# Kernel tuning notes

Measured on AMD Instinct MI355X. Metric: run time of the kernel, lower is better.

## Reference

```python
import jax, jax.numpy as jnp
import numpy as np

B, C, V, L = 64, 32, 1024, 12
C_OUT = 64
ORDER = 2
C_CAT = (ORDER * 3 + 1) * C  # 224


def setup_inputs() -> dict:
    key = jax.random.key(0)
    ks = jax.random.split(key, 6)
    x = jax.random.normal(ks[0], (B, C, V, L), dtype=jnp.float32)
    # random non-negative adjacencies, row-normalized like diffusion supports
    def adj(k):
        a = jax.random.uniform(k, (V, V), dtype=jnp.float32)
        return a / jnp.sum(a, axis=1, keepdims=True)
    a0, a1, a2 = adj(ks[1]), adj(ks[2]), adj(ks[3])
    W = jax.random.normal(ks[4], (C_OUT, C_CAT), dtype=jnp.float32) * 0.05
    b = jax.random.normal(ks[5], (C_OUT,), dtype=jnp.float32) * 0.05
    return {"x": x, "a0": a0, "a1": a1, "a2": a2, "W": W, "b": b}


def reference(x, a0, a1, a2, W, b):
    # diffusion propagation: x[b,c,v,l] @ A[v,w] -> [b,c,w,l]
    def prop(z, A):
        return jnp.einsum('ncvl,vw->ncwl', z, A)

    out = [x]
    for A in (a0, a1, a2):
        x1 = prop(x, A)
        out.append(x1)
        x2 = prop(x1, A)  # order=2
        out.append(x2)
    h = jnp.concatenate(out, axis=1)  # [B, 7*C, V, L]
    # 1x1 conv == channel GEMM; dropout is identity at inference
    return jnp.einsum('ncvl,oc->novl', h, W) + b[None, :, None, None]
```

## Files before the change

### kernel.cpp

```cpp
#include <hip/hip_runtime.h>
#include <hip/hip_bf16.h>


typedef __attribute__((ext_vector_type(4))) float  f32x4;
typedef __attribute__((ext_vector_type(8))) short  s16x8;
typedef __attribute__((ext_vector_type(4))) short  s16x4;

__device__ inline short f2bf(float f) {
    unsigned u = __builtin_bit_cast(unsigned, f);
    unsigned r = (u + 0x7FFFu + ((u >> 16) & 1u)) >> 16;
    return (short)r;
}

__device__ inline f32x4 mfma16(s16x8 a, s16x8 b, f32x4 c) {
    return __builtin_amdgcn_mfma_f32_16x16x32_bf16(a, b, c, 0, 0, 0);
}

__device__ inline void gll16(const void* g, void* l) {
    __builtin_amdgcn_global_load_lds(
        (const __attribute__((address_space(1))) void*)g,
        (__attribute__((address_space(3))) void*)l, 16, 0, 0);
}

__global__ __launch_bounds__(256) void cast_x_v2(const float* __restrict__ x,
                                                 short* __restrict__ Xg) {
    __shared__ short Xl[12 * 1040];
    const int bc = blockIdx.x;
    const int t  = threadIdx.x;
    const float4* src = (const float4*)(x + (size_t)bc * 12288);
#pragma unroll
    for (int k = 0; k < 12; ++k) {
        int f4 = k * 256 + t;
        float4 v = src[f4];
        int f  = f4 * 4;
        int vi = f / 12;
        int li = f - vi * 12;
        float vals[4] = {v.x, v.y, v.z, v.w};
#pragma unroll
        for (int e = 0; e < 4; ++e) {
            Xl[li * 1040 + vi] = f2bf(vals[e]);
            if (++li == 12) { li = 0; ++vi; }
        }
    }
    __syncthreads();
#pragma unroll
    for (int k = 0; k < 6; ++k) {
        int ch = k * 256 + t;
        int l  = ch >> 7;
        int v8 = ch & 127;
        *(s16x8*)(Xg + ((size_t)bc * 12 + l) * 1024 + v8 * 8) =
            *(const s16x8*)&Xl[l * 1040 + v8 * 8];
    }
}

__global__ __launch_bounds__(256) void cast_a_v2(const float* __restrict__ a0,
                                                 const float* __restrict__ a1,
                                                 const float* __restrict__ a2,
                                                 short* __restrict__ Btall,
                                                 short* __restrict__ Ab) {
    __shared__ float tbuf[32][33];
    const int z = blockIdx.z;
    const float* A = (z == 0) ? a0 : ((z == 1) ? a1 : a2);
    const int v0 = blockIdx.x * 32;
    const int w0 = blockIdx.y * 32;
    const int tr = threadIdx.x >> 3;
    const int tc = (threadIdx.x & 7) << 2;
    float4 val = *(const float4*)&A[(size_t)(v0 + tr) * 1024 + w0 + tc];
    s16x4 sb;
    sb[0] = f2bf(val.x); sb[1] = f2bf(val.y); sb[2] = f2bf(val.z); sb[3] = f2bf(val.w);
    *(s16x4*)(Ab + (size_t)z * 1048576 + (size_t)(v0 + tr) * 1024 + w0 + tc) = sb;
    tbuf[tr][tc + 0] = val.x; tbuf[tr][tc + 1] = val.y;
    tbuf[tr][tc + 2] = val.z; tbuf[tr][tc + 3] = val.w;
    __syncthreads();
    s16x4 st;
#pragma unroll
    for (int i = 0; i < 4; ++i) st[i] = f2bf(tbuf[tc + i][tr]);
    *(s16x4*)(Btall + (size_t)(2 * z) * 1048576 + (size_t)(w0 + tr) * 1024 + v0 + tc) = st;
}

__global__ __launch_bounds__(256, 2) void gemm_bt(const short* __restrict__ Xb, long xz,
                                                  const short* __restrict__ Btb, long bz,
                                                  short* __restrict__ Cb, long cz,
                                                  int crow) {
    __shared__ __align__(16) short Alds[128 * 32];
    __shared__ __align__(16) short Blds[128 * 32];

    const int tid  = threadIdx.x;
    const int lane = tid & 63;
    const int wid  = tid >> 6;
    const int wm   = wid >> 1;
    const int wn   = wid & 1;
    const int m0   = blockIdx.y * 128;
    const int n0   = blockIdx.x * 128;

    const short* X  = Xb  + (size_t)blockIdx.z * xz;
    const short* Bt = Btb + (size_t)blockIdx.z * bz;
    short*       C  = Cb  + (size_t)blockIdx.z * cz;

    const short* Ag = X  + (size_t)(m0 + wid * 32 + (lane >> 2)) * 1024 + (lane & 3) * 8;
    const short* Bg = Bt + (size_t)(n0 + wid * 32 + (lane >> 2)) * 1024 + (lane & 3) * 8;
    short* la = &Alds[wid * 1024];
    short* lb = &Blds[wid * 1024];

    const int lane15 = lane & 15;
    const int lq     = lane >> 4;
    const int ar     = lane15 * 32 + lq * 8;

    f32x4 acc[4][4] = {};

    for (int k0 = 0; k0 < 1024; k0 += 32) {
        __syncthreads();
        gll16(Ag + k0, la);
        gll16(Ag + k0 + 16 * 1024, la + 512);
        gll16(Bg + k0, lb);
        gll16(Bg + k0 + 16 * 1024, lb + 512);
        __syncthreads();

        s16x8 af[4], bf[4];
#pragma unroll
        for (int i = 0; i < 4; ++i)
            af[i] = *(const s16x8*)&Alds[(wm * 64 + i * 16) * 32 + ar];
#pragma unroll
        for (int j = 0; j < 4; ++j)
            bf[j] = *(const s16x8*)&Blds[(wn * 64 + j * 16) * 32 + ar];
#pragma unroll
        for (int i = 0; i < 4; ++i)
#pragma unroll
            for (int j = 0; j < 4; ++j)
                acc[i][j] = mfma16(af[i], bf[j], acc[i][j]);
    }

#pragma unroll
    for (int i = 0; i < 4; ++i) {
        int rbase = m0 + wm * 64 + i * 16 + lq * 4;
#pragma unroll
        for (int r = 0; r < 4; ++r) {
            size_t rowoff = (size_t)(rbase + r) * crow;
#pragma unroll
            for (int j = 0; j < 4; ++j) {
                int col = n0 + wn * 64 + j * 16 + lane15;
                C[rowoff + col] = f2bf(acc[i][j][r]);
            }
        }
    }
}


#define SB0   __builtin_amdgcn_sched_barrier(0)
#define BARM  asm volatile("s_barrier" ::: "memory")
#define LGKM0 asm volatile("s_waitcnt lgkmcnt(0)" ::: "memory")

#define STAGE_A(d, h, kt) do {                                               \
    const short* _s = Agp + (h) * 65536 + (kt) * 64;                         \
    short* _l = lA + (((d) * 2 + (h)) << 13);                                \
    gll16(_s, _l);                                                           \
    gll16(_s + 131072, _l + 4096);                                           \
} while (0)

#define STAGE_B(d, h, kt) do {                                               \
    const short* _s = Bgp + (h) * 32768 + (kt) * 64;                         \
    short* _l = lB + (((d) * 2 + (h)) << 13);                                \
    gll16(_s, _l);                                                           \
    gll16(_s + 131072, _l + 4096);                                           \
} while (0)

#define RD_A(D, MH) do {                                                     \
    const short* _p = Als + (((D) * 2 + (MH)) << 13) + aBase;                \
    _Pragma("unroll")                                                        \
    for (int _fm = 0; _fm < 4; ++_fm) {                                      \
        af[_fm][0] = *(const s16x8*)(_p + _fm * 1024 + slot0);               \
        af[_fm][1] = *(const s16x8*)(_p + _fm * 1024 + (slot0 ^ 32));        \
    }                                                                        \
} while (0)

#define RD_B(D, NH, dst) do {                                                \
    const short* _p = Bls + (((D) * 2 + (NH)) << 13) + bBase;                \
    _Pragma("unroll")                                                        \
    for (int _fn = 0; _fn < 2; ++_fn) {                                      \
        dst[_fn][0] = *(const s16x8*)(_p + _fn * 1024 + slot0);              \
        dst[_fn][1] = *(const s16x8*)(_p + _fn * 1024 + (slot0 ^ 32));       \
    }                                                                        \
} while (0)

#define MM(MH, NH, bv) do {                                                  \
    __builtin_amdgcn_s_setprio(1);                                           \
    _Pragma("unroll")                                                        \
    for (int _fm = 0; _fm < 4; ++_fm) {                                      \
        _Pragma("unroll")                                                    \
        for (int _fn = 0; _fn < 2; ++_fn) {                                  \
            _Pragma("unroll")                                                \
            for (int _kk = 0; _kk < 2; ++_kk)                                \
                acc[(MH) * 4 + _fm][(NH) * 2 + _fn] =                        \
                    mfma16(af[_fm][_kk], bv[_fn][_kk],                       \
                           acc[(MH) * 4 + _fm][(NH) * 2 + _fn]);             \
        }                                                                    \
    }                                                                        \
    __builtin_amdgcn_s_setprio(0);                                           \
} while (0)

#define VM4 asm volatile("s_waitcnt vmcnt(4)" ::: "memory")
#define VM0 asm volatile("s_waitcnt vmcnt(0)" ::: "memory")

#define TILE(D, T, S1, S2, VMST) do {                                        \
                                                             \
    RD_A(D, 0); RD_B(D, 0, bv0);                                             \
    if (S1) STAGE_A(1 - (D), 1, (T) + 1);                                    \
    SB0; BARM; SB0; LGKM0; SB0;                                              \
    MM(0, 0, bv0);                                                           \
    SB0; BARM; SB0;                                                          \
                                                             \
    RD_B(D, 1, bv1);                                                         \
    if (S1) STAGE_B(1 - (D), 1, (T) + 1);                                    \
    SB0; BARM; SB0; LGKM0; SB0;                                              \
    MM(0, 1, bv1);                                                           \
    SB0; BARM; SB0;                                                          \
                                                             \
    RD_A(D, 1);                                                              \
    if (S2) STAGE_A((D), 0, (T) + 2);                                        \
    SB0; BARM; SB0; LGKM0; SB0;                                              \
    MM(1, 1, bv1);                                                           \
    SB0; BARM; SB0;                                                          \
                                                             \
    if (S2) STAGE_B((D), 0, (T) + 2);                                        \
    SB0; BARM; SB0;                                                          \
    MM(1, 0, bv0);                                                           \
    SB0; VMST; BARM; SB0;                                                    \
} while (0)

__global__ __launch_bounds__(512, 2) void gemm256(const short* __restrict__ X,
                                                  const short* __restrict__ Bt,
                                                  short* __restrict__ C) {
    __shared__ __align__(16) short Als[32768];
    __shared__ __align__(16) short Bls[32768];

    const int t    = threadIdx.x;
    const int lane = t & 63;
    const int w    = t >> 6;
    const int wm   = w >> 2;
    const int wn   = w & 3;
    const int r15  = lane & 15;
    const int q    = lane >> 4;
    const int m0   = blockIdx.y << 8;
    const int n0   = blockIdx.x << 8;

    const int srow = t >> 3;
    const int kc8  = (((t & 7) - srow) & 7) * 8;
    const short* Agp = X + (size_t)(m0 + srow) * 1024 + kc8;
    const int rB0  = ((srow >> 5) << 6) | (srow & 31);
    const short* Bgp = Bt + (size_t)(n0 + rB0) * 1024 + kc8;
    short* lA = Als + t * 8;
    short* lB = Bls + t * 8;

    const int slot0 = ((q + r15) & 7) * 8;
    const int aBase = (wm * 64 + r15) * 64;
    const int bBase = (wn * 32 + r15) * 64;

    f32x4 acc[8][4] = {};
    s16x8 af[4][2], bv0[2][2], bv1[2][2];

    STAGE_A(0, 0, 0); STAGE_A(0, 1, 0); STAGE_B(0, 0, 0); STAGE_B(0, 1, 0);
    STAGE_A(1, 0, 1); STAGE_B(1, 0, 1);
    VM4;
    BARM; SB0;

#pragma unroll 1
    for (int it = 0; it < 7; ++it) {
        const int T = it * 2;
        TILE(0, T,     true, true, VM4);
        TILE(1, T + 1, true, true, VM4);
    }
    TILE(0, 14, true,  false, VM0);
    TILE(1, 15, false, false, (void)0);

#pragma unroll
    for (int fmt = 0; fmt < 8; ++fmt) {
        const int rbase = m0 + wm * 128 + fmt * 16 + q * 4;
#pragma unroll
        for (int r = 0; r < 4; ++r) {
            size_t rowoff = (size_t)(rbase + r) * 6144;
#pragma unroll
            for (int fnt = 0; fnt < 4; ++fnt) {
                int col = n0 + wn * 64 + fnt * 16 + r15;
                C[rowoff + col] = f2bf(acc[fmt][fnt][r]);
            }
        }
    }
}

__global__ __launch_bounds__(256, 2) void final_gemm2(const float* __restrict__ x,
                                                      const short* __restrict__ H,
                                                      const float* __restrict__ W,
                                                      const float* __restrict__ bias,
                                                      float* __restrict__ out) {
    __shared__ __align__(16) short Wl[64 * 40];
    __shared__ __align__(16) short Hl[384 * 40];

    const int t  = threadIdx.x;
    const int lane = t & 63;
    const int wv   = t >> 6;
    const int lane15 = lane & 15;
    const int lq     = lane >> 4;
    const int n  = blockIdx.y;
    const int v0 = blockIdx.x * 32;
    const int p0 = v0 * 12;

    const int hc    = t & 31;
    const int hw    = t >> 5;
    const int l_lo  = hw & 1;
    const int lane4 = hw >> 1;

    f32x4 acc[4][6] = {};

    for (int g = 0; g < 7; ++g) {
        __syncthreads();
        {
            int o = t >> 2, c0 = (t & 3) * 8;
            const float* wp = W + (size_t)o * 224 + g * 32 + c0;
            float4 w0 = *(const float4*)wp;
            float4 w1 = *(const float4*)(wp + 4);
            short* d = &Wl[o * 40 + c0];
            d[0] = f2bf(w0.x); d[1] = f2bf(w0.y); d[2] = f2bf(w0.z); d[3] = f2bf(w0.w);
            d[4] = f2bf(w1.x); d[5] = f2bf(w1.y); d[6] = f2bf(w1.z); d[7] = f2bf(w1.w);
        }
        if (g == 0) {
            int c = t >> 3, j0 = t & 7;
            const float* src = x + ((size_t)n * 32 + c) * 12288 + p0;
#pragma unroll
            for (int it = 0; it < 12; ++it) {
                int ch = j0 + it * 8;
                float4 v = *(const float4*)(src + ch * 4);
                int p = ch * 4;
                Hl[(p + 0) * 40 + c] = f2bf(v.x);
                Hl[(p + 1) * 40 + c] = f2bf(v.y);
                Hl[(p + 2) * 40 + c] = f2bf(v.z);
                Hl[(p + 3) * 40 + c] = f2bf(v.w);
            }
        } else {
            const short* base = H + (size_t)(g - 1) * 1024 + v0 + lane4 * 8;
#pragma unroll
            for (int lt = 0; lt < 6; ++lt) {
                int l = l_lo + 2 * lt;
                size_t row = ((size_t)n * 32 + hc) * 12 + l;
                s16x8 h8 = *(const s16x8*)(base + row * 6144);
#pragma unroll
                for (int i = 0; i < 8; ++i)
                    Hl[((lane4 * 8 + i) * 12 + l) * 40 + hc] = h8[i];
            }
        }
        __syncthreads();

        s16x8 af[4], bf[6];
#pragma unroll
        for (int ot = 0; ot < 4; ++ot)
            af[ot] = *(const s16x8*)&Wl[(ot * 16 + lane15) * 40 + lq * 8];
#pragma unroll
        for (int bt = 0; bt < 6; ++bt)
            bf[bt] = *(const s16x8*)&Hl[(wv * 96 + bt * 16 + lane15) * 40 + lq * 8];
#pragma unroll
        for (int ot = 0; ot < 4; ++ot)
#pragma unroll
            for (int bt = 0; bt < 6; ++bt)
                acc[ot][bt] = mfma16(af[ot], bf[bt], acc[ot][bt]);
    }

#pragma unroll
    for (int ot = 0; ot < 4; ++ot) {
#pragma unroll
        for (int r = 0; r < 4; ++r) {
            int o = ot * 16 + lq * 4 + r;
            float bo = bias[o];
            float* op = out + ((size_t)n * 64 + o) * 12288 + p0;
#pragma unroll
            for (int bt = 0; bt < 6; ++bt) {
                int p = wv * 96 + bt * 16 + lane15;
                op[p] = acc[ot][bt][r] + bo;
            }
        }
    }
}

extern "C" void kernel_launch(void* const* d_in, const int* in_sizes, int n_in,
                              void* d_out, int out_size, void* d_ws, size_t ws_size,
                              hipStream_t stream) {
    const float* x  = (const float*)d_in[0];
    const float* a0 = (const float*)d_in[1];
    const float* a1 = (const float*)d_in[2];
    const float* a2 = (const float*)d_in[3];
    const float* W  = (const float*)d_in[4];
    const float* bs = (const float*)d_in[5];
    float* out = (float*)d_out;

    char* ws = (char*)d_ws;
    short* Xg    = (short*)(ws);
    short* Ab    = (short*)(ws + 50331648L);
    short* Btall = (short*)(ws + 56623104L);
    short* Hmv   = (short*)(ws + 69206016L);

    cast_x_v2<<<2048, 256, 0, stream>>>(x, Xg);
    cast_a_v2<<<dim3(32, 32, 3), 256, 0, stream>>>(a0, a1, a2, Btall, Ab);

    gemm_bt<<<dim3(8, 8, 3), 256, 0, stream>>>(
        Btall, 2097152L, Ab, 1048576L, Btall + 1048576L, 2097152L, 1024);

    gemm256<<<dim3(24, 96), 512, 0, stream>>>(Xg, Btall, Hmv);

    final_gemm2<<<dim3(32, 64), 256, 0, stream>>>(x, Hmv, W, bs, out);
}
```

Baseline: 792.6 us.

## Write propagation output channel-contiguous and pipeline final channel GEMM with async LDS loads

The big propagation GEMM now writes its output in a [b, v, l, 192-channel] layout, and the input cast reorders rows to (b, l, c), so the final 1x1-conv GEMM can read contiguous channel rows. The final kernel is rewritten: it loads all of W once, stages H tiles with global_load_lds into a swizzled triple buffer, and overlaps loads with MFMA across the 7 channel groups. This removes the strided, transposing loads and per-group syncs of the old final kernel. The cost is scattered 8-byte stores in the big GEMM epilogue and more LDS per block.

```diff
diff --git a/kernel.cpp b/kernel.cpp
--- a/kernel.cpp
+++ b/kernel.cpp
@@ -21,12 +21,18 @@
         (const __attribute__((address_space(1))) void*)g,
         (__attribute__((address_space(3))) void*)l, 16, 0, 0);
 }
+
+#define SB0   __builtin_amdgcn_sched_barrier(0)
+#define BARM  asm volatile("s_barrier" ::: "memory")
+#define LGKM0 asm volatile("s_waitcnt lgkmcnt(0)" ::: "memory")
 
 __global__ __launch_bounds__(256) void cast_x_v2(const float* __restrict__ x,
                                                  short* __restrict__ Xg) {
     __shared__ short Xl[12 * 1040];
     const int bc = blockIdx.x;
     const int t  = threadIdx.x;
+    const int b  = bc >> 5;
+    const int c  = bc & 31;
     const float4* src = (const float4*)(x + (size_t)bc * 12288);
 #pragma unroll
     for (int k = 0; k < 12; ++k) {
@@ -48,7 +54,7 @@
         int ch = k * 256 + t;
         int l  = ch >> 7;
         int v8 = ch & 127;
-        *(s16x8*)(Xg + ((size_t)bc * 12 + l) * 1024 + v8 * 8) =
+        *(s16x8*)(Xg + (size_t)(b * 384 + l * 32 + c) * 1024 + v8 * 8) =
             *(const s16x8*)&Xl[l * 1040 + v8 * 8];
     }
 }
@@ -145,10 +151,6 @@
     }
 }
 
-
-#define SB0   __builtin_amdgcn_sched_barrier(0)
-#define BARM  asm volatile("s_barrier" ::: "memory")
-#define LGKM0 asm volatile("s_waitcnt lgkmcnt(0)" ::: "memory")
 
 #define STAGE_A(d, h, kt) do {                                               \
     const short* _s = Agp + (h) * 65536 + (kt) * 64;                         \
@@ -272,109 +274,145 @@
     TILE(0, 14, true,  false, VM0);
     TILE(1, 15, false, false, (void)0);
 
+    const int s_idx  = n0 >> 10;
+    const int v_base = (n0 & 1023) + wn * 64 + r15;
+    const int ks0    = s_idx * 32 + q * 4;
 #pragma unroll
     for (int fmt = 0; fmt < 8; ++fmt) {
-        const int rbase = m0 + wm * 128 + fmt * 16 + q * 4;
-#pragma unroll
-        for (int r = 0; r < 4; ++r) {
-            size_t rowoff = (size_t)(rbase + r) * 6144;
-#pragma unroll
-            for (int fnt = 0; fnt < 4; ++fnt) {
-                int col = n0 + wn * 64 + fnt * 16 + r15;
-                C[rowoff + col] = f2bf(acc[fmt][fnt][r]);
-            }
-        }
-    }
-}
-
-__global__ __launch_bounds__(256, 2) void final_gemm2(const float* __restrict__ x,
-                                                      const short* __restrict__ H,
-                                                      const float* __restrict__ W,
-                                                      const float* __restrict__ bias,
-                                                      float* __restrict__ out) {
-    __shared__ __align__(16) short Wl[64 * 40];
-    __shared__ __align__(16) short Hl[384 * 40];
-
-    const int t  = threadIdx.x;
+        const int gidx = (m0 >> 5) + wm * 4 + (fmt >> 1);
+        const int bb   = gidx / 12;
+        const int ll   = gidx - bb * 12;
+        const int ks   = ks0 + (fmt & 1) * 16;
+        const size_t base = (size_t)bb * 12288 + ll;
+#pragma unroll
+        for (int fnt = 0; fnt < 4; ++fnt) {
+            const int v = v_base + fnt * 16;
+            s16x4 sv;
+            sv[0] = f2bf(acc[fmt][fnt][0]);
+            sv[1] = f2bf(acc[fmt][fnt][1]);
+            sv[2] = f2bf(acc[fmt][fnt][2]);
+            sv[3] = f2bf(acc[fmt][fnt][3]);
+            *(s16x4*)(C + (base + (size_t)v * 12) * 192 + ks) = sv;
+        }
+    }
+}
+
+__global__ __launch_bounds__(256, 2) void gemm_fin(const float* __restrict__ x,
+                                                   const short* __restrict__ Hc,
+                                                   const float* __restrict__ W,
+                                                   const float* __restrict__ bias,
+                                                   float* __restrict__ out) {
+    __shared__ __align__(16) short Wl[64 * 232];
+    __shared__ __align__(16) short Hl[3][8192];
+
+    const int t    = threadIdx.x;
     const int lane = t & 63;
     const int wv   = t >> 6;
-    const int lane15 = lane & 15;
-    const int lq     = lane >> 4;
-    const int n  = blockIdx.y;
-    const int v0 = blockIdx.x * 32;
-    const int p0 = v0 * 12;
-
-    const int hc    = t & 31;
-    const int hw    = t >> 5;
-    const int l_lo  = hw & 1;
-    const int lane4 = hw >> 1;
-
-    f32x4 acc[4][6] = {};
-
-    for (int g = 0; g < 7; ++g) {
-        __syncthreads();
-        {
-            int o = t >> 2, c0 = (t & 3) * 8;
-            const float* wp = W + (size_t)o * 224 + g * 32 + c0;
-            float4 w0 = *(const float4*)wp;
-            float4 w1 = *(const float4*)(wp + 4);
-            short* d = &Wl[o * 40 + c0];
-            d[0] = f2bf(w0.x); d[1] = f2bf(w0.y); d[2] = f2bf(w0.z); d[3] = f2bf(w0.w);
-            d[4] = f2bf(w1.x); d[5] = f2bf(w1.y); d[6] = f2bf(w1.z); d[7] = f2bf(w1.w);
-        }
-        if (g == 0) {
-            int c = t >> 3, j0 = t & 7;
-            const float* src = x + ((size_t)n * 32 + c) * 12288 + p0;
-#pragma unroll
-            for (int it = 0; it < 12; ++it) {
-                int ch = j0 + it * 8;
-                float4 v = *(const float4*)(src + ch * 4);
-                int p = ch * 4;
-                Hl[(p + 0) * 40 + c] = f2bf(v.x);
-                Hl[(p + 1) * 40 + c] = f2bf(v.y);
-                Hl[(p + 2) * 40 + c] = f2bf(v.z);
-                Hl[(p + 3) * 40 + c] = f2bf(v.w);
+    const int r15  = lane & 15;
+    const int lq   = lane >> 4;
+    const int blk  = blockIdx.x;
+    const int b    = blk / 48;
+    const int p0   = (blk - b * 48) * 256;
+    const size_t R0 = (size_t)b * 12288 + p0;
+
+    {
+        const int o  = t >> 2;
+        const int c0 = (t & 3) * 56;
+        const float* wp = W + o * 224 + c0;
+        short* d = &Wl[o * 232 + c0];
+#pragma unroll
+        for (int i = 0; i < 14; ++i) {
+            float4 w4 = *(const float4*)(wp + i * 4);
+            s16x4 s;
+            s[0] = f2bf(w4.x); s[1] = f2bf(w4.y); s[2] = f2bf(w4.z); s[3] = f2bf(w4.w);
+            *(s16x4*)(d + i * 4) = s;
+        }
+    }
+    {
+        const int c  = t & 31;
+        const int pc = t >> 5;
+        const float* xp = x + ((size_t)b * 32 + c) * 12288 + p0 + pc * 32;
+        const int kc = c >> 3, ko = c & 7;
+#pragma unroll
+        for (int j4 = 0; j4 < 8; ++j4) {
+            float4 v = *(const float4*)(xp + j4 * 4);
+            float vals[4] = {v.x, v.y, v.z, v.w};
+#pragma unroll
+            for (int e = 0; e < 4; ++e) {
+                int row = pc * 32 + j4 * 4 + e;
+                Hl[0][row * 32 + (((kc + (row >> 1)) & 3) << 3) + ko] = f2bf(vals[e]);
             }
-        } else {
-            const short* base = H + (size_t)(g - 1) * 1024 + v0 + lane4 * 8;
-#pragma unroll
-            for (int lt = 0; lt < 6; ++lt) {
-                int l = l_lo + 2 * lt;
-                size_t row = ((size_t)n * 32 + hc) * 12 + l;
-                s16x8 h8 = *(const s16x8*)(base + row * 6144);
-#pragma unroll
-                for (int i = 0; i < 8; ++i)
-                    Hl[((lane4 * 8 + i) * 12 + l) * 40 + hc] = h8[i];
-            }
-        }
-        __syncthreads();
-
-        s16x8 af[4], bf[6];
-#pragma unroll
-        for (int ot = 0; ot < 4; ++ot)
-            af[ot] = *(const s16x8*)&Wl[(ot * 16 + lane15) * 40 + lq * 8];
-#pragma unroll
-        for (int bt = 0; bt < 6; ++bt)
-            bf[bt] = *(const s16x8*)&Hl[(wv * 96 + bt * 16 + lane15) * 40 + lq * 8];
-#pragma unroll
-        for (int ot = 0; ot < 4; ++ot)
-#pragma unroll
-            for (int bt = 0; bt < 6; ++bt)
-                acc[ot][bt] = mfma16(af[ot], bf[bt], acc[ot][bt]);
-    }
+        }
+    }
+    const int grow = t >> 2;
+    const int slot = t & 3;
+#define GLLSTEP(step, buf) do {                                              \
+    _Pragma("unroll")                                                        \
+    for (int _i = 0; _i < 4; ++_i) {                                         \
+        int _row = _i * 64 + grow;                                           \
+        int _kc  = (slot - (_row >> 1)) & 3;                                 \
+        gll16(Hc + (R0 + _row) * 192 + ((step) - 1) * 32 + _kc * 8,          \
+              &Hl[buf][(_i * 256 + t) * 8]);                                 \
+    }                                                                        \
+} while (0)
+
+    GLLSTEP(1, 1);
+    GLLSTEP(2, 2);
+    LGKM0;
+    BARM; SB0;
+
+    f32x4 acc[4][4] = {};
+
+#define FINSTEP(s, buf) do {                                                 \
+    s16x8 af[4], bfr[4];                                                     \
+    _Pragma("unroll")                                                        \
+    for (int _ot = 0; _ot < 4; ++_ot)                                        \
+        af[_ot] = *(const s16x8*)&Wl[(_ot * 16 + r15) * 232 + (s) * 32 + lq * 8]; \
+    _Pragma("unroll")                                                        \
+    for (int _bt = 0; _bt < 4; ++_bt) {                                      \
+        int _row = wv * 64 + _bt * 16 + r15;                                 \
+        bfr[_bt] = *(const s16x8*)&Hl[buf][_row * 32 + ((((lq) + (_row >> 1)) & 3) << 3)]; \
+    }                                                                        \
+    _Pragma("unroll")                                                        \
+    for (int _ot = 0; _ot < 4; ++_ot) {                                      \
+        _Pragma("unroll")                                                    \
+        for (int _bt = 0; _bt < 4; ++_bt)                                    \
+            acc[_ot][_bt] = mfma16(af[_ot], bfr[_bt], acc[_ot][_bt]);        \
+    }                                                                        \
+} while (0)
+
+#define VMW(n) asm volatile("s_waitcnt vmcnt(" #n ")" ::: "memory")
+
+    FINSTEP(0, 0);
+    BARM; SB0; GLLSTEP(3, 0);
+    VMW(8); BARM; SB0;
+    FINSTEP(1, 1);
+    BARM; SB0; GLLSTEP(4, 1);
+    VMW(8); BARM; SB0;
+    FINSTEP(2, 2);
+    BARM; SB0; GLLSTEP(5, 2);
+    VMW(8); BARM; SB0;
+    FINSTEP(3, 0);
+    BARM; SB0; GLLSTEP(6, 0);
+    VMW(8); BARM; SB0;
+    FINSTEP(4, 1);
+    BARM; SB0;
+    VMW(4); BARM; SB0;
+    FINSTEP(5, 2);
+    BARM; SB0;
+    VMW(0); BARM; SB0;
+    FINSTEP(6, 0);
 
 #pragma unroll
     for (int ot = 0; ot < 4; ++ot) {
 #pragma unroll
         for (int r = 0; r < 4; ++r) {
-            int o = ot * 16 + lq * 4 + r;
-            float bo = bias[o];
-            float* op = out + ((size_t)n * 64 + o) * 12288 + p0;
-#pragma unroll
-            for (int bt = 0; bt < 6; ++bt) {
-                int p = wv * 96 + bt * 16 + lane15;
-                op[p] = acc[ot][bt][r] + bo;
-            }
+            const int o = ot * 16 + lq * 4 + r;
+            const float bo = bias[o];
+            float* op = out + ((size_t)b * 64 + o) * 12288 + p0;
+#pragma unroll
+            for (int bt = 0; bt < 4; ++bt)
+                op[wv * 64 + bt * 16 + r15] = acc[ot][bt][r] + bo;
         }
     }
 }
@@ -394,7 +432,7 @@
     short* Xg    = (short*)(ws);
     short* Ab    = (short*)(ws + 50331648L);
     short* Btall = (short*)(ws + 56623104L);
-    short* Hmv   = (short*)(ws + 69206016L);
+    short* Hcat  = (short*)(ws + 69206016L);
 
     cast_x_v2<<<2048, 256, 0, stream>>>(x, Xg);
     cast_a_v2<<<dim3(32, 32, 3), 256, 0, stream>>>(a0, a1, a2, Btall, Ab);
@@ -402,7 +440,7 @@
     gemm_bt<<<dim3(8, 8, 3), 256, 0, stream>>>(
         Btall, 2097152L, Ab, 1048576L, Btall + 1048576L, 2097152L, 1024);
 
-    gemm256<<<dim3(24, 96), 512, 0, stream>>>(Xg, Btall, Hmv);
-
-    final_gemm2<<<dim3(32, 64), 256, 0, stream>>>(x, Hmv, W, bs, out);
-}
+    gemm256<<<dim3(24, 96), 512, 0, stream>>>(Xg, Btall, Hcat);
+
+    gemm_fin<<<3072, 256, 0, stream>>>(x, Hcat, W, bs, out);
+}
```

After: 745.8 us. -5.9%, faster.
